# Optimization experiments

Measured on AMD Instinct MI355X. Metric: run time of the kernel, lower is better.

The kernel has to match this reference:

```python
import jax, jax.numpy as jnp
import numpy as np

B, N, D_IN, D_OUT, H = 4, 2048, 1024, 1024, 16
HEAD_DIM = D_OUT // H


def setup_inputs() -> dict:
    key = jax.random.key(0)
    k1, k2, k3 = jax.random.split(key, 3)
    x = jax.random.normal(k1, (B, N, D_IN), dtype=jnp.float32)
    # torch Linear: y = x @ W.T + b; we store W already transposed as [in, out]
    w_attn = jax.random.normal(k2, (D_IN, 3 * D_OUT), dtype=jnp.float32) * (1.0 / np.sqrt(D_IN))
    w_proj = jax.random.normal(k3, (D_OUT, D_OUT), dtype=jnp.float32) * (1.0 / np.sqrt(D_OUT))
    b_proj = jnp.zeros((D_OUT,), dtype=jnp.float32)
    return {"x": x, "w_attn": w_attn, "w_proj": w_proj, "b_proj": b_proj}


def reference(x, w_attn, w_proj, b_proj):
    b, n, _ = x.shape
    qkv = x @ w_attn  # [b, n, 3*d_out]
    q, k, v = jnp.split(qkv, 3, axis=2)
    # [b, n, d_out] -> [b, h, n, head_dim]
    def to_heads(t):
        return t.reshape(b, n, H, HEAD_DIM).transpose(0, 2, 1, 3)
    q, k, v = to_heads(q), to_heads(k), to_heads(v)
    scale = 1.0 / np.sqrt(HEAD_DIM).astype(np.float32)
    att = jnp.einsum('bhqd,bhkd->bhqk', q, k) * scale  # [b, h, n, n]
    causal = jnp.tril(jnp.ones((n, n), dtype=bool))  # True = keep
    att = jnp.where(causal, att, -jnp.inf)
    att = jax.nn.softmax(att, axis=-1)
    # dropout p=0.0 -> identity
    out = jnp.einsum('bhqk,bhkd->bhqd', att, v)  # [b, h, n, head_dim]
    out = out.transpose(0, 2, 1, 3).reshape(b, n, D_OUT)
    return out @ w_proj + b_proj
```

## Files before the change

kernel.cpp:

```cpp
#include <hip/hip_runtime.h>
#include <hip/hip_bf16.h>
#include <stdint.h>

typedef short short8 __attribute__((ext_vector_type(8)));
typedef float f32x4 __attribute__((ext_vector_type(4)));

#define BQ 4
#define NSEQ 2048
#define DMODEL 1024
#define NHEAD 16
#define HDIM 64
#define MTOT 8192
#define QKV_LD 3072

#if __has_builtin(__builtin_amdgcn_exp2f)
#define EXP2(x) __builtin_amdgcn_exp2f(x)
#else
#define EXP2(x) exp2f(x)
#endif
#define C_SCL 0.18033688f
#define THR_RAW 16.635532f

__device__ __forceinline__ uint16_t f2bf(float f) {
  uint32_t u = __builtin_bit_cast(uint32_t, f);
  uint32_t r = (u + 0x7FFFu + ((u >> 16) & 1u)) >> 16;
  return (uint16_t)r;
}
__device__ __forceinline__ uint16_t f2bf_hw(float f) {
  __hip_bfloat16 h = __float2bfloat16(f);
  return __builtin_bit_cast(uint16_t, h);
}

__global__ void prep_k(const float* __restrict__ x, uint16_t* __restrict__ xb,
                       const float* __restrict__ w_attn, uint16_t* __restrict__ wat,
                       const float* __restrict__ w_proj, uint16_t* __restrict__ wpt) {
  __shared__ float tile[32][33];
  const int bid = blockIdx.x;
  if (bid < 2048) {
    int idx = (bid * 256 + threadIdx.x) * 4;
    const int stride = 2048 * 256 * 4;
    for (int i = idx; i < MTOT * DMODEL; i += stride) {
      float4 v = *reinterpret_cast<const float4*>(x + i);
      ushort4 o;
      o.x = f2bf(v.x); o.y = f2bf(v.y); o.z = f2bf(v.z); o.w = f2bf(v.w);
      *reinterpret_cast<ushort4*>(xb + i) = o;
    }
    return;
  }
  const float* in; uint16_t* out; int N, t;
  if (bid < 2048 + 3072) { in = w_attn; out = wat; N = 3072; t = bid - 2048; }
  else                   { in = w_proj; out = wpt; N = 1024; t = bid - 5120; }
  const int K = 1024;
  const int nb = N / 32;
  const int n0 = (t % nb) * 32;
  const int k0 = (t / nb) * 32;
  const int tx = threadIdx.x & 31;
  const int ty = threadIdx.x >> 5;
#pragma unroll
  for (int r = 0; r < 4; ++r)
    tile[ty + r * 8][tx] = in[(size_t)(k0 + ty + r * 8) * N + n0 + tx];
  __syncthreads();
#pragma unroll
  for (int r = 0; r < 4; ++r)
    out[(size_t)(n0 + ty + r * 8) * K + k0 + tx] = f2bf(tile[tx][ty + r * 8]);
}

template <bool BF16_OUT>
__global__ void __launch_bounds__(256, 3)
gemm_bt_k(const uint16_t* __restrict__ A, const uint16_t* __restrict__ BT,
          void* __restrict__ Cout, const float* __restrict__ bias,
          int M, int N, int K) {
  __shared__ uint16_t As[128 * 32];
  __shared__ uint16_t Bs[128 * 32];
  const int tid = threadIdx.x;
  const int lane = tid & 63;
  const int wave = tid >> 6;
  const int wr = wave >> 1, wc = wave & 1;
  const int brow = blockIdx.y * 128;
  const int bcol = blockIdx.x * 128;
  const int l16 = lane & 15;
  const int lq = lane >> 4;

  f32x4 acc[4][4];
  const f32x4 fzero = {0.f, 0.f, 0.f, 0.f};
#pragma unroll
  for (int i = 0; i < 4; ++i)
#pragma unroll
    for (int j = 0; j < 4; ++j) acc[i][j] = fzero;

  const int ca = tid, cb = tid + 256;
  const size_t ga0 = (size_t)(brow + (ca >> 2)) * K + (ca & 3) * 8;
  const size_t ga1 = (size_t)(brow + (cb >> 2)) * K + (cb & 3) * 8;
  const size_t gb0 = (size_t)(bcol + (ca >> 2)) * K + (ca & 3) * 8;
  const size_t gb1 = (size_t)(bcol + (cb >> 2)) * K + (cb & 3) * 8;

  for (int kt = 0; kt < K; kt += 32) {
    __builtin_amdgcn_global_load_lds(
        (const __attribute__((address_space(1))) void*)(A + ga0 + kt),
        (__attribute__((address_space(3))) void*)&As[ca * 8], 16, 0, 0);
    __builtin_amdgcn_global_load_lds(
        (const __attribute__((address_space(1))) void*)(A + ga1 + kt),
        (__attribute__((address_space(3))) void*)&As[cb * 8], 16, 0, 0);
    __builtin_amdgcn_global_load_lds(
        (const __attribute__((address_space(1))) void*)(BT + gb0 + kt),
        (__attribute__((address_space(3))) void*)&Bs[ca * 8], 16, 0, 0);
    __builtin_amdgcn_global_load_lds(
        (const __attribute__((address_space(1))) void*)(BT + gb1 + kt),
        (__attribute__((address_space(3))) void*)&Bs[cb * 8], 16, 0, 0);
    __syncthreads();
    short8 af[4], bfr[4];
#pragma unroll
    for (int r = 0; r < 4; ++r) {
      af[r]  = *reinterpret_cast<const short8*>(&As[(wr * 64 + r * 16 + l16) * 32 + lq * 8]);
      bfr[r] = *reinterpret_cast<const short8*>(&Bs[(wc * 64 + r * 16 + l16) * 32 + lq * 8]);
    }
#pragma unroll
    for (int r = 0; r < 4; ++r)
#pragma unroll
      for (int c = 0; c < 4; ++c)
        acc[r][c] = __builtin_amdgcn_mfma_f32_16x16x32_bf16(af[r], bfr[c], acc[r][c], 0, 0, 0);
    __syncthreads();
  }

#pragma unroll
  for (int r = 0; r < 4; ++r) {
    const int row0 = brow + wr * 64 + r * 16 + lq * 4;
#pragma unroll
    for (int c = 0; c < 4; ++c) {
      const int col = bcol + wc * 64 + c * 16 + l16;
#pragma unroll
      for (int i = 0; i < 4; ++i) {
        if constexpr (BF16_OUT)
          reinterpret_cast<uint16_t*>(Cout)[(size_t)(row0 + i) * N + col] = f2bf(acc[r][c][i]);
        else
          reinterpret_cast<float*>(Cout)[(size_t)(row0 + i) * N + col] = acc[r][c][i] + bias[col];
      }
    }
  }
}

__global__ void __launch_bounds__(256, 3)
attn_fwd_k(const uint16_t* __restrict__ qkv, uint16_t* __restrict__ outb) {
  const int obid = blockIdx.x;
  const int bid = (obid & 7) * 128 + (obid >> 3);
  const int p = bid & 15;
  const int h = (bid >> 4) & 15;
  const int b = bid >> 8;
  const int qtA = p;
  const int qtB = 31 - p;
  const int tid = threadIdx.x;
  const int lane = tid & 63;
  const int w = tid >> 6;
  const int l16 = lane & 15;
  const int lq = lane >> 4;

  __shared__ uint16_t Ks[64 * 72];
  __shared__ uint16_t Vt[64 * 72];

  short8 qaA0, qaA1, qaB0, qaB1;
  {
    const size_t baseA = ((size_t)(b * NSEQ + qtA * 64 + w * 16 + l16)) * QKV_LD + h * 64 + lq * 8;
    const size_t baseB = ((size_t)(b * NSEQ + qtB * 64 + w * 16 + l16)) * QKV_LD + h * 64 + lq * 8;
    qaA0 = *reinterpret_cast<const short8*>(qkv + baseA);
    qaA1 = *reinterpret_cast<const short8*>(qkv + baseA + 32);
    qaB0 = *reinterpret_cast<const short8*>(qkv + baseB);
    qaB1 = *reinterpret_cast<const short8*>(qkv + baseB + 32);
  }

  float mA = -1e30f, lA = 0.f, mB = -1e30f, lB = 0.f;
  f32x4 accA[4], accB[4];
  const f32x4 fzero = {0.f, 0.f, 0.f, 0.f};
#pragma unroll
  for (int i = 0; i < 4; ++i) { accA[i] = fzero; accB[i] = fzero; }

  const int r0 = tid >> 3, d0 = (tid & 7) * 8;
  const int ka0 = r0 * 72 + d0;
  const int ka1 = (r0 + 32) * 72 + d0;
  const int lqt = (r0 >> 2) & 3;
  const int nc0 = r0 >> 4;
  const int m0 = d0 >> 3;
  const int jo = (nc0 & 1) * 4 + (r0 & 3);
  const int vcol0 = (((2 * lqt) ^ m0) * 8) + jo;
  const int vcol1 = (((2 * lqt + 1) ^ m0) * 8) + jo;

  const int ntiles = qtB + 1;
  short8 rk0, rk1, rv0, rv1;
  {
    const size_t g0 = ((size_t)(b * NSEQ + r0)) * QKV_LD + 1024 + h * 64 + d0;
    const size_t g1 = ((size_t)(b * NSEQ + r0 + 32)) * QKV_LD + 1024 + h * 64 + d0;
    rk0 = *reinterpret_cast<const short8*>(qkv + g0);
    rv0 = *reinterpret_cast<const short8*>(qkv + g0 + 1024);
    rk1 = *reinterpret_cast<const short8*>(qkv + g1);
    rv1 = *reinterpret_cast<const short8*>(qkv + g1 + 1024);
  }

#define SOFTMAX_PV(SV, M_I, L_I, ACC, DIAG)                                     \
  {                                                                             \
    float tmax_ = -3e38f;                                                       \
    if (DIAG) {                                                                 \
      _Pragma("unroll") for (int nc = 0; nc < 4; ++nc) {                        \
        _Pragma("unroll") for (int i = 0; i < 4; ++i) {                         \
          float v_ = SV[nc][i];                                                 \
          if ((nc * 16 + lq * 4 + i) > (w * 16 + l16)) v_ = -3e38f;             \
          SV[nc][i] = v_;                                                       \
          tmax_ = fmaxf(tmax_, v_);                                             \
        }                                                                       \
      }                                                                         \
    } else {                                                                    \
      _Pragma("unroll") for (int nc = 0; nc < 4; ++nc)                          \
        tmax_ = fmaxf(tmax_, fmaxf(fmaxf(SV[nc][0], SV[nc][1]),                 \
                                   fmaxf(SV[nc][2], SV[nc][3])));               \
    }                                                                           \
    tmax_ = fmaxf(tmax_, __shfl_xor(tmax_, 16, 64));                            \
    tmax_ = fmaxf(tmax_, __shfl_xor(tmax_, 32, 64));                            \
    if (!__all(tmax_ <= M_I + THR_RAW)) {                                       \
      const float mn_ = fmaxf(M_I, tmax_);                                      \
      const float alpha_ = EXP2((M_I - mn_) * C_SCL);                           \
      M_I = mn_;                                                                \
      L_I *= alpha_;                                                            \
      float ab_[4];                                                             \
      _Pragma("unroll") for (int i = 0; i < 4; ++i)                             \
        ab_[i] = __shfl(alpha_, lq * 4 + i, 64);                                \
      _Pragma("unroll") for (int d4 = 0; d4 < 4; ++d4)                          \
        _Pragma("unroll") for (int i = 0; i < 4; ++i)                           \
          ACC[d4][i] *= ab_[i];                                                 \
    }                                                                           \
    const float mc_ = M_I * C_SCL;                                              \
    float rsum_ = 0.f;                                                          \
    short8 pa0_, pa1_;                                                          \
    _Pragma("unroll") for (int nc = 0; nc < 4; ++nc) {                          \
      _Pragma("unroll") for (int i = 0; i < 4; ++i) {                           \
        float pv_ = EXP2(__builtin_fmaf(SV[nc][i], C_SCL, -mc_));               \
        rsum_ += pv_;                                                           \
        uint16_t ph_ = f2bf_hw(pv_);                                            \
        if (nc < 2) pa0_[nc * 4 + i] = (short)ph_;                              \
        else        pa1_[(nc - 2) * 4 + i] = (short)ph_;                        \
      }                                                                         \
    }                                                                           \
    rsum_ += __shfl_xor(rsum_, 16, 64);                                         \
    rsum_ += __shfl_xor(rsum_, 32, 64);                                         \
    L_I += rsum_;                                                               \
    _Pragma("unroll") for (int d4 = 0; d4 < 4; ++d4) {                          \
      const int drow_ = d4 * 16 + l16;                                          \
      const int xr_ = (drow_ >> 3) & 7;                                         \
      short8 vb0_ = *reinterpret_cast<const short8*>(&Vt[drow_ * 72 + (((2 * lq) ^ xr_) * 8)]); \
      short8 vb1_ = *reinterpret_cast<const short8*>(&Vt[drow_ * 72 + (((2 * lq + 1) ^ xr_) * 8)]); \
      ACC[d4] = __builtin_amdgcn_mfma_f32_16x16x32_bf16(pa0_, vb0_, ACC[d4], 0, 0, 0); \
      ACC[d4] = __builtin_amdgcn_mfma_f32_16x16x32_bf16(pa1_, vb1_, ACC[d4], 0, 0, 0); \
    }                                                                           \
  }

  for (int jt = 0; jt < ntiles; ++jt) {
    *reinterpret_cast<short8*>(&Ks[ka0]) = rk0;
    *reinterpret_cast<short8*>(&Ks[ka1]) = rk1;
#pragma unroll
    for (int j = 0; j < 8; ++j) Vt[(d0 + j) * 72 + vcol0] = (uint16_t)rv0[j];
#pragma unroll
    for (int j = 0; j < 8; ++j) Vt[(d0 + j) * 72 + vcol1] = (uint16_t)rv1[j];
    if (jt + 1 < ntiles) {
      const size_t g0 = ((size_t)(b * NSEQ + (jt + 1) * 64 + r0)) * QKV_LD + 1024 + h * 64 + d0;
      const size_t g1 = ((size_t)(b * NSEQ + (jt + 1) * 64 + r0 + 32)) * QKV_LD + 1024 + h * 64 + d0;
      rk0 = *reinterpret_cast<const short8*>(qkv + g0);
      rv0 = *reinterpret_cast<const short8*>(qkv + g0 + 1024);
      rk1 = *reinterpret_cast<const short8*>(qkv + g1);
      rv1 = *reinterpret_cast<const short8*>(qkv + g1 + 1024);
    }
    __syncthreads();

    {
      f32x4 sv[4];
#pragma unroll
      for (int nc = 0; nc < 4; ++nc) {
        short8 kb0 = *reinterpret_cast<const short8*>(&Ks[(nc * 16 + l16) * 72 + lq * 8]);
        short8 kb1 = *reinterpret_cast<const short8*>(&Ks[(nc * 16 + l16) * 72 + 32 + lq * 8]);
        f32x4 s = fzero;
        s = __builtin_amdgcn_mfma_f32_16x16x32_bf16(kb0, qaB0, s, 0, 0, 0);
        s = __builtin_amdgcn_mfma_f32_16x16x32_bf16(kb1, qaB1, s, 0, 0, 0);
        sv[nc] = s;
      }
      SOFTMAX_PV(sv, mB, lB, accB, jt == qtB);
    }

    if (jt <= qtA) {
      f32x4 sv[4];
#pragma unroll
      for (int nc = 0; nc < 4; ++nc) {
        short8 kb0 = *reinterpret_cast<const short8*>(&Ks[(nc * 16 + l16) * 72 + lq * 8]);
        short8 kb1 = *reinterpret_cast<const short8*>(&Ks[(nc * 16 + l16) * 72 + 32 + lq * 8]);
        f32x4 s = fzero;
        s = __builtin_amdgcn_mfma_f32_16x16x32_bf16(kb0, qaA0, s, 0, 0, 0);
        s = __builtin_amdgcn_mfma_f32_16x16x32_bf16(kb1, qaA1, s, 0, 0, 0);
        sv[nc] = s;
      }
      SOFTMAX_PV(sv, mA, lA, accA, jt == qtA);
    }

    __syncthreads();
  }

  {
    float lb4[4];
#pragma unroll
    for (int i = 0; i < 4; ++i) lb4[i] = __shfl(lA, lq * 4 + i, 64);
    const size_t orow = (size_t)(b * NSEQ) + qtA * 64 + w * 16 + lq * 4;
#pragma unroll
    for (int d4 = 0; d4 < 4; ++d4)
#pragma unroll
      for (int i = 0; i < 4; ++i)
        outb[(orow + i) * (size_t)DMODEL + h * 64 + d4 * 16 + l16] = f2bf_hw(accA[d4][i] / lb4[i]);
  }
  {
    float lb4[4];
#pragma unroll
    for (int i = 0; i < 4; ++i) lb4[i] = __shfl(lB, lq * 4 + i, 64);
    const size_t orow = (size_t)(b * NSEQ) + qtB * 64 + w * 16 + lq * 4;
#pragma unroll
    for (int d4 = 0; d4 < 4; ++d4)
#pragma unroll
      for (int i = 0; i < 4; ++i)
        outb[(orow + i) * (size_t)DMODEL + h * 64 + d4 * 16 + l16] = f2bf_hw(accB[d4][i] / lb4[i]);
  }
}

extern "C" void kernel_launch(void* const* d_in, const int* in_sizes, int n_in,
                              void* d_out, int out_size, void* d_ws, size_t ws_size,
                              hipStream_t stream) {
  const float* x      = (const float*)d_in[0];
  const float* w_attn = (const float*)d_in[1];
  const float* w_proj = (const float*)d_in[2];
  const float* b_proj = (const float*)d_in[3];

  uint16_t* xb    = (uint16_t*)d_ws;
  uint16_t* wat   = xb   + (size_t)MTOT * DMODEL;
  uint16_t* wpt   = wat  + (size_t)3072 * 1024;
  uint16_t* qkvb  = wpt  + (size_t)1024 * 1024;
  uint16_t* attnb = qkvb + (size_t)MTOT * QKV_LD;

  prep_k<<<2048 + 3072 + 1024, 256, 0, stream>>>(x, xb, w_attn, wat, w_proj, wpt);

  gemm_bt_k<true><<<dim3(3072 / 128, MTOT / 128), 256, 0, stream>>>(
      xb, wat, qkvb, nullptr, MTOT, 3072, 1024);

  attn_fwd_k<<<BQ * NHEAD * 16, 256, 0, stream>>>(qkvb, attnb);

  gemm_bt_k<false><<<dim3(1024 / 128, MTOT / 128), 256, 0, stream>>>(
      attnb, wpt, d_out, b_proj, MTOT, 1024, 1024);
}
```

Baseline: 187.7 us.

## Double GEMM K-tile to 64 with XOR-swizzled LDS layout

The GEMM kernel now stages a 64-wide K slice per iteration instead of 32, which halves the number of barrier pairs per output tile. The LDS placement is XOR-swizzled through the global source addresses so that the short8 fragment reads avoid bank conflicts. The bf16 epilogue switches to a hardware conversion helper, f2bf_hw. LDS use per block doubles, which may reduce occupancy, and f2bf_hw must be defined in the part of the file not shown.

```diff
diff --git a/kernel.cpp b/kernel.cpp
--- a/kernel.cpp
+++ b/kernel.cpp
@@ -70,8 +70,8 @@
 gemm_bt_k(const uint16_t* __restrict__ A, const uint16_t* __restrict__ BT,
           void* __restrict__ Cout, const float* __restrict__ bias,
           int M, int N, int K) {
-  __shared__ uint16_t As[128 * 32];
-  __shared__ uint16_t Bs[128 * 32];
+  __shared__ uint16_t As[128 * 64];
+  __shared__ uint16_t Bs[128 * 64];
   const int tid = threadIdx.x;
   const int lane = tid & 63;
   const int wave = tid >> 6;
@@ -88,39 +88,55 @@
 #pragma unroll
     for (int j = 0; j < 4; ++j) acc[i][j] = fzero;
 
-  const int ca = tid, cb = tid + 256;
-  const size_t ga0 = (size_t)(brow + (ca >> 2)) * K + (ca & 3) * 8;
-  const size_t ga1 = (size_t)(brow + (cb >> 2)) * K + (cb & 3) * 8;
-  const size_t gb0 = (size_t)(bcol + (ca >> 2)) * K + (ca & 3) * 8;
-  const size_t gb1 = (size_t)(bcol + (cb >> 2)) * K + (cb & 3) * 8;
-
-  for (int kt = 0; kt < K; kt += 32) {
-    __builtin_amdgcn_global_load_lds(
-        (const __attribute__((address_space(1))) void*)(A + ga0 + kt),
-        (__attribute__((address_space(3))) void*)&As[ca * 8], 16, 0, 0);
-    __builtin_amdgcn_global_load_lds(
-        (const __attribute__((address_space(1))) void*)(A + ga1 + kt),
-        (__attribute__((address_space(3))) void*)&As[cb * 8], 16, 0, 0);
-    __builtin_amdgcn_global_load_lds(
-        (const __attribute__((address_space(1))) void*)(BT + gb0 + kt),
-        (__attribute__((address_space(3))) void*)&Bs[ca * 8], 16, 0, 0);
-    __builtin_amdgcn_global_load_lds(
-        (const __attribute__((address_space(1))) void*)(BT + gb1 + kt),
-        (__attribute__((address_space(3))) void*)&Bs[cb * 8], 16, 0, 0);
+  size_t gA0, gA1, gA2, gA3, gB0, gB1, gB2, gB3;
+  int ls0, ls1, ls2, ls3;
+  {
+    int c0 = tid, c1 = tid + 256, c2 = tid + 512, c3 = tid + 768;
+    int r0 = c0 >> 3, r1 = c1 >> 3, r2 = c2 >> 3, r3 = c3 >> 3;
+    int k0 = (c0 & 7) ^ (r0 & 7), k1 = (c1 & 7) ^ (r1 & 7);
+    int k2 = (c2 & 7) ^ (r2 & 7), k3 = (c3 & 7) ^ (r3 & 7);
+    gA0 = (size_t)(brow + r0) * K + k0 * 8;  gB0 = (size_t)(bcol + r0) * K + k0 * 8;
+    gA1 = (size_t)(brow + r1) * K + k1 * 8;  gB1 = (size_t)(bcol + r1) * K + k1 * 8;
+    gA2 = (size_t)(brow + r2) * K + k2 * 8;  gB2 = (size_t)(bcol + r2) * K + k2 * 8;
+    gA3 = (size_t)(brow + r3) * K + k3 * 8;  gB3 = (size_t)(bcol + r3) * K + k3 * 8;
+    ls0 = c0 * 8; ls1 = c1 * 8; ls2 = c2 * 8; ls3 = c3 * 8;
+  }
+
+#define GLD(PTR, OFF, LDSARR, LS)                                               \
+  __builtin_amdgcn_global_load_lds(                                             \
+      (const __attribute__((address_space(1))) void*)((PTR) + (OFF)),           \
+      (__attribute__((address_space(3))) void*)&LDSARR[LS], 16, 0, 0)
+
+  for (int kt = 0; kt < K; kt += 64) {
+    GLD(A, gA0 + kt, As, ls0);
+    GLD(A, gA1 + kt, As, ls1);
+    GLD(A, gA2 + kt, As, ls2);
+    GLD(A, gA3 + kt, As, ls3);
+    GLD(BT, gB0 + kt, Bs, ls0);
+    GLD(BT, gB1 + kt, Bs, ls1);
+    GLD(BT, gB2 + kt, Bs, ls2);
+    GLD(BT, gB3 + kt, Bs, ls3);
     __syncthreads();
-    short8 af[4], bfr[4];
-#pragma unroll
-    for (int r = 0; r < 4; ++r) {
-      af[r]  = *reinterpret_cast<const short8*>(&As[(wr * 64 + r * 16 + l16) * 32 + lq * 8]);
-      bfr[r] = *reinterpret_cast<const short8*>(&Bs[(wc * 64 + r * 16 + l16) * 32 + lq * 8]);
-    }
-#pragma unroll
-    for (int r = 0; r < 4; ++r)
-#pragma unroll
-      for (int c = 0; c < 4; ++c)
-        acc[r][c] = __builtin_amdgcn_mfma_f32_16x16x32_bf16(af[r], bfr[c], acc[r][c], 0, 0, 0);
+#pragma unroll
+    for (int kk = 0; kk < 2; ++kk) {
+      short8 af[4], bfr[4];
+#pragma unroll
+      for (int r = 0; r < 4; ++r) {
+        const int rowA = wr * 64 + r * 16 + l16;
+        const int rowB = wc * 64 + r * 16 + l16;
+        const int slot = (kk * 4 + lq) ^ (l16 & 7);
+        af[r]  = *reinterpret_cast<const short8*>(&As[rowA * 64 + slot * 8]);
+        bfr[r] = *reinterpret_cast<const short8*>(&Bs[rowB * 64 + slot * 8]);
+      }
+#pragma unroll
+      for (int r = 0; r < 4; ++r)
+#pragma unroll
+        for (int c = 0; c < 4; ++c)
+          acc[r][c] = __builtin_amdgcn_mfma_f32_16x16x32_bf16(af[r], bfr[c], acc[r][c], 0, 0, 0);
+    }
     __syncthreads();
   }
+#undef GLD
 
 #pragma unroll
   for (int r = 0; r < 4; ++r) {
@@ -131,7 +147,7 @@
 #pragma unroll
       for (int i = 0; i < 4; ++i) {
         if constexpr (BF16_OUT)
-          reinterpret_cast<uint16_t*>(Cout)[(size_t)(row0 + i) * N + col] = f2bf(acc[r][c][i]);
+          reinterpret_cast<uint16_t*>(Cout)[(size_t)(row0 + i) * N + col] = f2bf_hw(acc[r][c][i]);
         else
           reinterpret_cast<float*>(Cout)[(size_t)(row0 + i) * N + col] = acc[r][c][i] + bias[col];
       }
```

Result: faster. 180.0 us (-4.1%).
